# Kernel optimization log

Measured on AMD Instinct MI355X. Metric: run time of the kernel, lower is better.

Reference implementation:

```python
import jax, jax.numpy as jnp
import numpy as np

N, E, V_IN, HID, U_IN, B, MEM = 50000, 800000, 128, 128, 64, 64, 128
CAT = V_IN + HID + U_IN  # 320 == hidden*2 + u_in
ALPHA = 0.5
EPS = 1e-5


def setup_inputs() -> dict:
    key = jax.random.key(0)
    ks = jax.random.split(key, 12)
    x = jax.random.normal(ks[0], (N, V_IN), dtype=jnp.float32)
    edge_index = jax.random.randint(ks[1], (2, E), 0, N, dtype=jnp.int64)
    edge_attr = jax.random.normal(ks[2], (E, HID), dtype=jnp.float32)
    u = jax.random.normal(ks[3], (B, U_IN), dtype=jnp.float32)
    batch = jnp.sort(jax.random.randint(ks[4], (N,), 0, B, dtype=jnp.int64))
    Mk = jax.random.normal(ks[5], (MEM, CAT), dtype=jnp.float32)
    Mv = jax.random.normal(ks[6], (MEM, CAT), dtype=jnp.float32)
    ln_gamma = jnp.ones((CAT,), dtype=jnp.float32)
    ln_beta = jnp.zeros((CAT,), dtype=jnp.float32)
    W1 = jax.random.normal(ks[7], (CAT, HID), dtype=jnp.float32) * (1.0 / np.sqrt(CAT))
    b1 = jnp.zeros((HID,), dtype=jnp.float32)
    W2 = jax.random.normal(ks[8], (HID, HID), dtype=jnp.float32) * (1.0 / np.sqrt(HID))
    b2 = jnp.zeros((HID,), dtype=jnp.float32)
    return {"x": x, "edge_index": edge_index, "edge_attr": edge_attr, "u": u,
            "batch": batch, "Mk": Mk, "Mv": Mv, "ln_gamma": ln_gamma,
            "ln_beta": ln_beta, "W1": W1, "b1": b1, "W2": W2, "b2": b2}


def reference(x, edge_index, edge_attr, u, batch, Mk, Mv, ln_gamma, ln_beta, W1, b1, W2, b2):
    # scatter_add over destination nodes
    agg = jax.ops.segment_sum(edge_attr, edge_index[1], num_segments=N)  # [N, HID]
    out = jnp.concatenate([x, agg, u[batch]], axis=1)  # [N, CAT]
    # LayerNorm over last dim
    mu = jnp.mean(out, axis=-1, keepdims=True)
    var = jnp.var(out, axis=-1, keepdims=True)
    out = (out - mu) * jax.lax.rsqrt(var + EPS) * ln_gamma + ln_beta
    # External attention: [N,CAT] @ [CAT,MEM] -> softmax over MEM -> @ [MEM,CAT]
    scores = jnp.einsum('nc,mc->nm', out, Mk)
    attn = jax.nn.softmax(scores, axis=-1)
    attn_out = jnp.einsum('nm,mc->nc', attn, Mv)
    out = ALPHA * attn_out + (1.0 - ALPHA) * out
    # MLP
    h = jax.nn.relu(out @ W1 + b1)
    return h @ W2 + b2
```

## Files before the change

### kernel.cpp

```cpp
#include <hip/hip_runtime.h>

#define NN   50000
#define EE   800000
#define VIN  128
#define HIDN 128
#define UIN  64
#define MEMN 128
#define CATN 320
#define LN_EPS 1e-5f
#define SCAN_NB 196

typedef __attribute__((ext_vector_type(8))) short short8;
typedef __attribute__((ext_vector_type(4))) float f32x4;
typedef __attribute__((ext_vector_type(4))) unsigned int uint4v;
typedef unsigned short ushort_t;

__device__ inline ushort_t f32_bf16(float f) {
    unsigned u = __float_as_uint(f);
    return (ushort_t)((u + 0x7FFFu + ((u >> 16) & 1u)) >> 16);
}
__device__ inline float bf16_f32(ushort_t h) {
    return __uint_as_float(((unsigned)h) << 16);
}
__device__ inline unsigned pack_hl(float y) {
    unsigned u  = __float_as_uint(y);
    unsigned hi = (u + 0x7FFFu + ((u >> 16) & 1u)) & 0xFFFF0000u;
    float    lo = y - __uint_as_float(hi);
    unsigned v  = __float_as_uint(lo);
    unsigned l16 = ((v + 0x7FFFu + ((v >> 16) & 1u)) >> 16) & 0xFFFFu;
    return hi | l16;
}

__global__ void hist_kernel(const int* __restrict__ edge_dst, int* __restrict__ count)
{
    int gid = blockIdx.x * 256 + threadIdx.x;
    if (gid < EE) atomicAdd(&count[edge_dst[gid]], 1);
}

__global__ void block_sum_kernel(const int* __restrict__ count, int* __restrict__ partials)
{
    __shared__ int s[256];
    const int tid = threadIdx.x;
    const int gid = blockIdx.x * 256 + tid;
    s[tid] = (gid < NN) ? count[gid] : 0;
    __syncthreads();
    for (int off = 128; off >= 1; off >>= 1) {
        if (tid < off) s[tid] += s[tid + off];
        __syncthreads();
    }
    if (tid == 0) partials[blockIdx.x] = s[0];
}

__global__ void scan_partials_kernel(int* __restrict__ partials)
{
    __shared__ int s[256];
    const int tid = threadIdx.x;
    const int v = (tid < SCAN_NB) ? partials[tid] : 0;
    s[tid] = v;
    __syncthreads();
    for (int off = 1; off < 256; off <<= 1) {
        int t = (tid >= off) ? s[tid - off] : 0;
        __syncthreads();
        s[tid] += t;
        __syncthreads();
    }
    if (tid < SCAN_NB) partials[tid] = s[tid] - v;
}

__global__ void make_offsets_kernel(const int* __restrict__ count,
                                    const int* __restrict__ partials,
                                    int* __restrict__ offsets)
{
    __shared__ int s[256];
    const int tid = threadIdx.x;
    const int gid = blockIdx.x * 256 + tid;
    const int v = (gid < NN) ? count[gid] : 0;
    s[tid] = v;
    __syncthreads();
    for (int off = 1; off < 256; off <<= 1) {
        int t = (tid >= off) ? s[tid - off] : 0;
        __syncthreads();
        s[tid] += t;
        __syncthreads();
    }
    if (gid < NN) offsets[gid] = partials[blockIdx.x] + s[tid] - v;
}

__global__ void fill_kernel(const int* __restrict__ edge_dst,
                            const int* __restrict__ offsets,
                            int* __restrict__ cursor,
                            int* __restrict__ bucket)
{
    int gid = blockIdx.x * 256 + threadIdx.x;
    if (gid >= EE) return;
    const int d = edge_dst[gid];
    const int p = atomicAdd(&cursor[d], 1);
    bucket[offsets[d] + p] = gid;
}

__global__ __launch_bounds__(256) void gather_ln_kernel(
    const float* __restrict__ edge_attr,
    const int*   __restrict__ bucket,
    const int*   __restrict__ offsets,
    const int*   __restrict__ count,
    const float* __restrict__ x,
    const float* __restrict__ u,
    const int*   __restrict__ batch,
    const float* __restrict__ gamma,
    const float* __restrict__ beta,
    unsigned*    __restrict__ ln_pk)
{
    const int wid  = (blockIdx.x * 256 + threadIdx.x) >> 6;
    const int lane = threadIdx.x & 63;
    if (wid >= NN) return;

    const int start = offsets[wid];
    const int deg   = count[wid];
    float2 a = make_float2(0.f, 0.f);
    for (int i = 0; i < deg; ++i) {
        const int e = bucket[start + i];
        const float2 v = reinterpret_cast<const float2*>(edge_attr)[e * 64 + lane];
        a.x += v.x;
        a.y += v.y;
    }
    const float2 xv = reinterpret_cast<const float2*>(x)[(size_t)wid * 64 + lane];
    const float  uv = u[batch[wid] * UIN + lane];

    float s = xv.x + xv.y + a.x + a.y + uv;
    float q = xv.x * xv.x + xv.y * xv.y + a.x * a.x + a.y * a.y + uv * uv;
    #pragma unroll
    for (int off = 32; off >= 1; off >>= 1) {
        s += __shfl_xor(s, off);
        q += __shfl_xor(q, off);
    }
    const float mu  = s * (1.0f / CATN);
    const float var = q * (1.0f / CATN) - mu * mu;
    const float rs  = rsqrtf(var + LN_EPS);

    const float2 g0 = reinterpret_cast<const float2*>(gamma)[lane];
    const float2 g1 = reinterpret_cast<const float2*>(gamma)[64 + lane];
    const float  g2 = gamma[256 + lane];
    const float2 t0 = reinterpret_cast<const float2*>(beta)[lane];
    const float2 t1 = reinterpret_cast<const float2*>(beta)[64 + lane];
    const float  t2 = beta[256 + lane];

    unsigned* row = ln_pk + (size_t)wid * CATN;
    uint2 p01, p23;
    p01.x = pack_hl((xv.x - mu) * rs * g0.x + t0.x);
    p01.y = pack_hl((xv.y - mu) * rs * g0.y + t0.y);
    p23.x = pack_hl((a.x - mu) * rs * g1.x + t1.x);
    p23.y = pack_hl((a.y - mu) * rs * g1.y + t1.y);
    reinterpret_cast<uint2*>(row)[lane]       = p01;
    reinterpret_cast<uint2*>(row + 128)[lane] = p23;
    row[256 + lane] = pack_hl((uv - mu) * rs * g2 + t2);
}

__global__ void prep_mk_kernel(const float* __restrict__ Mk,
                               ushort_t* __restrict__ mk_hi, ushort_t* __restrict__ mk_lo)
{
    int i = blockIdx.x * 256 + threadIdx.x;
    if (i < MEMN * CATN) {
        const float f = Mk[i];
        const ushort_t h = f32_bf16(f);
        mk_hi[i] = h;
        mk_lo[i] = f32_bf16(f - bf16_f32(h));
    }
}
__global__ void prep_mvt_kernel(const float* __restrict__ Mv, ushort_t* __restrict__ mv_t)
{
    int i = blockIdx.x * 256 + threadIdx.x;
    if (i < CATN * MEMN) {
        int c = i >> 7, m = i & 127;
        mv_t[i] = f32_bf16(Mv[m * CATN + c]);
    }
}
__global__ void prep_w1t_kernel(const float* __restrict__ W1, ushort_t* __restrict__ w1_t)
{
    int i = blockIdx.x * 256 + threadIdx.x;
    if (i < HIDN * CATN) {
        int n = i / CATN, k = i - n * CATN;
        w1_t[i] = f32_bf16(W1[k * HIDN + n]);
    }
}
__global__ void prep_w2t_kernel(const float* __restrict__ W2, ushort_t* __restrict__ w2_t)
{
    int i = blockIdx.x * 256 + threadIdx.x;
    if (i < HIDN * HIDN) {
        int n = i >> 7, k = i & 127;
        w2_t[i] = f32_bf16(W2[k * HIDN + n]);
    }
}

#define MSTR 328
#define SSTR 132
#define PSTR 136

__global__ __launch_bounds__(256) void node_mfma_kernel(
    const unsigned* __restrict__ ln_pk,
    const ushort_t* __restrict__ mk_hi,
    const ushort_t* __restrict__ mk_lo,
    const ushort_t* __restrict__ mv_t,
    const ushort_t* __restrict__ w1_t,
    const ushort_t* __restrict__ w2_t,
    const float*    __restrict__ b1,
    const float*    __restrict__ b2,
    float*          __restrict__ out)
{
    __shared__ __align__(16) ushort_t s_lnh[32 * MSTR];
    __shared__ __align__(16) ushort_t s_lnl[32 * MSTR];
    __shared__ __align__(16) float    s_S[32 * SSTR];
    __shared__ __align__(16) ushort_t s_P[32 * PSTR];

    const int tid  = threadIdx.x;
    const int wv   = tid >> 6;
    const int lane = tid & 63;
    const int l15  = lane & 15;
    const int l4   = lane >> 4;
    const int node0 = blockIdx.x * 32;

    const f32x4 zero4 = {0.f, 0.f, 0.f, 0.f};

    for (int j = tid; j < 32 * 80; j += 256) {
        const int nl = j / 80;
        const int c0 = (j - nl * 80) * 4;
        int ng = node0 + nl; ng = (ng < NN) ? ng : (NN - 1);
        const uint4v p = *(const uint4v*)(ln_pk + (size_t)ng * CATN + c0);
        ushort_t* ph = s_lnh + nl * MSTR + c0;
        ushort_t* pl = s_lnl + nl * MSTR + c0;
        ph[0] = (ushort_t)(p.x >> 16);  pl[0] = (ushort_t)(p.x & 0xFFFFu);
        ph[1] = (ushort_t)(p.y >> 16);  pl[1] = (ushort_t)(p.y & 0xFFFFu);
        ph[2] = (ushort_t)(p.z >> 16);  pl[2] = (ushort_t)(p.z & 0xFFFFu);
        ph[3] = (ushort_t)(p.w >> 16);  pl[3] = (ushort_t)(p.w & 0xFFFFu);
    }
    __syncthreads();

    {
        f32x4 acc[2][2];
        #pragma unroll
        for (int mt = 0; mt < 2; ++mt)
            #pragma unroll
            for (int nt = 0; nt < 2; ++nt) acc[mt][nt] = zero4;

        for (int kc = 0; kc < 10; ++kc) {
            const int koff = kc * 32 + l4 * 8;
            short8 ah[2], al[2], bh[2], bl[2];
            #pragma unroll
            for (int mt = 0; mt < 2; ++mt) {
                ah[mt] = *(const short8*)(s_lnh + (mt * 16 + l15) * MSTR + koff);
                al[mt] = *(const short8*)(s_lnl + (mt * 16 + l15) * MSTR + koff);
            }
            #pragma unroll
            for (int nt = 0; nt < 2; ++nt) {
                const int mr = (wv * 2 + nt) * 16 + l15;
                bh[nt] = *(const short8*)(mk_hi + (size_t)mr * CATN + koff);
                bl[nt] = *(const short8*)(mk_lo + (size_t)mr * CATN + koff);
            }
            #pragma unroll
            for (int mt = 0; mt < 2; ++mt)
                #pragma unroll
                for (int nt = 0; nt < 2; ++nt) {
                    acc[mt][nt] = __builtin_amdgcn_mfma_f32_16x16x32_bf16(ah[mt], bh[nt], acc[mt][nt], 0, 0, 0);
                    acc[mt][nt] = __builtin_amdgcn_mfma_f32_16x16x32_bf16(ah[mt], bl[nt], acc[mt][nt], 0, 0, 0);
                    acc[mt][nt] = __builtin_amdgcn_mfma_f32_16x16x32_bf16(al[mt], bh[nt], acc[mt][nt], 0, 0, 0);
                }
        }
        #pragma unroll
        for (int mt = 0; mt < 2; ++mt)
            #pragma unroll
            for (int nt = 0; nt < 2; ++nt)
                #pragma unroll
                for (int r = 0; r < 4; ++r)
                    s_S[(mt * 16 + l4 * 4 + r) * SSTR + (wv * 2 + nt) * 16 + l15] = acc[mt][nt][r];
    }
    __syncthreads();

    {
        const int nd = tid >> 3, j = tid & 7;
        const float* row = s_S + nd * SSTR + j * 16;
        float vals[16];
        float mx = -1e30f;
        #pragma unroll
        for (int i = 0; i < 16; ++i) { vals[i] = row[i]; mx = fmaxf(mx, vals[i]); }
        mx = fmaxf(mx, __shfl_xor(mx, 1));
        mx = fmaxf(mx, __shfl_xor(mx, 2));
        mx = fmaxf(mx, __shfl_xor(mx, 4));
        float sm = 0.f;
        #pragma unroll
        for (int i = 0; i < 16; ++i) { vals[i] = __expf(vals[i] - mx); sm += vals[i]; }
        sm += __shfl_xor(sm, 1);
        sm += __shfl_xor(sm, 2);
        sm += __shfl_xor(sm, 4);
        const float inv = 1.f / sm;
        unsigned* prow = (unsigned*)(s_P + nd * PSTR + j * 16);
        #pragma unroll
        for (int i2 = 0; i2 < 8; ++i2) {
            unsigned pk = (unsigned)f32_bf16(vals[2 * i2] * inv) |
                          ((unsigned)f32_bf16(vals[2 * i2 + 1] * inv) << 16);
            prow[i2] = pk;
        }
    }
    __syncthreads();

    {
        f32x4 acc[2][5];
        #pragma unroll
        for (int mt = 0; mt < 2; ++mt)
            #pragma unroll
            for (int nn = 0; nn < 5; ++nn) acc[mt][nn] = zero4;

        for (int kc = 0; kc < 4; ++kc) {
            const int koff = kc * 32 + l4 * 8;
            short8 ap[2];
            #pragma unroll
            for (int mt = 0; mt < 2; ++mt)
                ap[mt] = *(const short8*)(s_P + (mt * 16 + l15) * PSTR + koff);
            short8 bv[5];
            #pragma unroll
            for (int nn = 0; nn < 5; ++nn) {
                const int c = (wv * 5 + nn) * 16 + l15;
                bv[nn] = *(const short8*)(mv_t + (size_t)c * MEMN + koff);
            }
            #pragma unroll
            for (int mt = 0; mt < 2; ++mt)
                #pragma unroll
                for (int nn = 0; nn < 5; ++nn)
                    acc[mt][nn] = __builtin_amdgcn_mfma_f32_16x16x32_bf16(ap[mt], bv[nn], acc[mt][nn], 0, 0, 0);
        }
        #pragma unroll
        for (int mt = 0; mt < 2; ++mt)
            #pragma unroll
            for (int nn = 0; nn < 5; ++nn)
                #pragma unroll
                for (int r = 0; r < 4; ++r) {
                    const int node_l = mt * 16 + l4 * 4 + r;
                    const int c = (wv * 5 + nn) * 16 + l15;
                    const int idx = node_l * MSTR + c;
                    const float lnv = bf16_f32(s_lnh[idx]) + bf16_f32(s_lnl[idx]);
                    s_lnh[idx] = f32_bf16(0.5f * (acc[mt][nn][r] + lnv));
                }
    }
    __syncthreads();

    {
        f32x4 acc[2][2];
        #pragma unroll
        for (int mt = 0; mt < 2; ++mt)
            #pragma unroll
            for (int nt = 0; nt < 2; ++nt) acc[mt][nt] = zero4;

        for (int kc = 0; kc < 10; ++kc) {
            const int koff = kc * 32 + l4 * 8;
            short8 am[2], bw[2];
            #pragma unroll
            for (int mt = 0; mt < 2; ++mt)
                am[mt] = *(const short8*)(s_lnh + (mt * 16 + l15) * MSTR + koff);
            #pragma unroll
            for (int nt = 0; nt < 2; ++nt) {
                const int n = (wv * 2 + nt) * 16 + l15;
                bw[nt] = *(const short8*)(w1_t + (size_t)n * CATN + koff);
            }
            #pragma unroll
            for (int mt = 0; mt < 2; ++mt)
                #pragma unroll
                for (int nt = 0; nt < 2; ++nt)
                    acc[mt][nt] = __builtin_amdgcn_mfma_f32_16x16x32_bf16(am[mt], bw[nt], acc[mt][nt], 0, 0, 0);
        }
        float bb[2];
        #pragma unroll
        for (int nt = 0; nt < 2; ++nt) bb[nt] = b1[(wv * 2 + nt) * 16 + l15];
        __syncthreads();
        #pragma unroll
        for (int mt = 0; mt < 2; ++mt)
            #pragma unroll
            for (int nt = 0; nt < 2; ++nt)
                #pragma unroll
                for (int r = 0; r < 4; ++r) {
                    const int node_l = mt * 16 + l4 * 4 + r;
                    const int col = (wv * 2 + nt) * 16 + l15;
                    s_P[node_l * PSTR + col] = f32_bf16(fmaxf(acc[mt][nt][r] + bb[nt], 0.f));
                }
    }
    __syncthreads();

    {
        f32x4 acc[2][2];
        #pragma unroll
        for (int mt = 0; mt < 2; ++mt)
            #pragma unroll
            for (int nt = 0; nt < 2; ++nt) acc[mt][nt] = zero4;

        for (int kc = 0; kc < 4; ++kc) {
            const int koff = kc * 32 + l4 * 8;
            short8 ah[2], bw[2];
            #pragma unroll
            for (int mt = 0; mt < 2; ++mt)
                ah[mt] = *(const short8*)(s_P + (mt * 16 + l15) * PSTR + koff);
            #pragma unroll
            for (int nt = 0; nt < 2; ++nt) {
                const int n = (wv * 2 + nt) * 16 + l15;
                bw[nt] = *(const short8*)(w2_t + (size_t)n * HIDN + koff);
            }
            #pragma unroll
            for (int mt = 0; mt < 2; ++mt)
                #pragma unroll
                for (int nt = 0; nt < 2; ++nt)
                    acc[mt][nt] = __builtin_amdgcn_mfma_f32_16x16x32_bf16(ah[mt], bw[nt], acc[mt][nt], 0, 0, 0);
        }
        float bb[2];
        #pragma unroll
        for (int nt = 0; nt < 2; ++nt) bb[nt] = b2[(wv * 2 + nt) * 16 + l15];
        #pragma unroll
        for (int mt = 0; mt < 2; ++mt)
            #pragma unroll
            for (int nt = 0; nt < 2; ++nt)
                #pragma unroll
                for (int r = 0; r < 4; ++r) {
                    const int ng = node0 + mt * 16 + l4 * 4 + r;
                    if (ng < NN) {
                        const int col = (wv * 2 + nt) * 16 + l15;
                        out[(size_t)ng * HIDN + col] = acc[mt][nt][r] + bb[nt];
                    }
                }
    }
}

extern "C" void kernel_launch(void* const* d_in, const int* in_sizes, int n_in,
                              void* d_out, int out_size, void* d_ws, size_t ws_size,
                              hipStream_t stream)
{
    const float* x         = (const float*)d_in[0];
    const int*   edge_idx  = (const int*)  d_in[1];
    const float* edge_attr = (const float*)d_in[2];
    const float* u         = (const float*)d_in[3];
    const int*   batch     = (const int*)  d_in[4];
    const float* Mk        = (const float*)d_in[5];
    const float* Mv        = (const float*)d_in[6];
    const float* gamma     = (const float*)d_in[7];
    const float* beta      = (const float*)d_in[8];
    const float* W1        = (const float*)d_in[9];
    const float* b1        = (const float*)d_in[10];
    const float* W2        = (const float*)d_in[11];
    const float* b2        = (const float*)d_in[12];
    float*       out       = (float*)d_out;

    char* w = (char*)d_ws;
    int*   count     = (int*)w;        w += (size_t)NN * sizeof(int);
    int*   cursor    = (int*)w;        w += (size_t)NN * sizeof(int);
    int*   offsets   = (int*)w;        w += (size_t)NN * sizeof(int);
    int*   partials  = (int*)w;        w += 256 * sizeof(int);
    int*   bucket    = (int*)w;        w += (size_t)EE * sizeof(int);
    w = (char*)(((size_t)w + 255) & ~(size_t)255);
    unsigned* ln_pk  = (unsigned*)w;   w += (size_t)NN * CATN * sizeof(unsigned);
    ushort_t* mk_hi  = (ushort_t*)w;   w += (size_t)MEMN * CATN * 2;
    ushort_t* mk_lo  = (ushort_t*)w;   w += (size_t)MEMN * CATN * 2;
    ushort_t* mv_t   = (ushort_t*)w;   w += (size_t)CATN * MEMN * 2;
    ushort_t* w1_t   = (ushort_t*)w;   w += (size_t)HIDN * CATN * 2;
    ushort_t* w2_t   = (ushort_t*)w;   w += (size_t)HIDN * HIDN * 2;

    const int* edge_dst = edge_idx + EE;

    hipMemsetAsync(count, 0, (size_t)2 * NN * sizeof(int), stream);

    const int eb = (EE + 255) / 256;
    hist_kernel<<<eb, 256, 0, stream>>>(edge_dst, count);
    block_sum_kernel<<<SCAN_NB, 256, 0, stream>>>(count, partials);
    scan_partials_kernel<<<1, 256, 0, stream>>>(partials);
    make_offsets_kernel<<<SCAN_NB, 256, 0, stream>>>(count, partials, offsets);
    fill_kernel<<<eb, 256, 0, stream>>>(edge_dst, offsets, cursor, bucket);

    prep_mk_kernel <<<(MEMN * CATN + 255) / 256, 256, 0, stream>>>(Mk, mk_hi, mk_lo);
    prep_mvt_kernel<<<(CATN * MEMN + 255) / 256, 256, 0, stream>>>(Mv, mv_t);
    prep_w1t_kernel<<<(HIDN * CATN + 255) / 256, 256, 0, stream>>>(W1, w1_t);
    prep_w2t_kernel<<<(HIDN * HIDN + 255) / 256, 256, 0, stream>>>(W2, w2_t);

    gather_ln_kernel<<<(NN * 64 + 255) / 256, 256, 0, stream>>>(
        edge_attr, bucket, offsets, count, x, u, batch, gamma, beta, ln_pk);

    node_mfma_kernel<<<(NN + 31) / 32, 256, 0, stream>>>(
        ln_pk, mk_hi, mk_lo, mv_t, w1_t, w2_t, b1, b2, out);
}
```

Measured before the change: 354.1 us.

## Unroll edge gather by four, vectorize LDS split stores, unroll MFMA k-loops

The edge aggregation loop in the gather/LayerNorm kernel is unrolled by four. This keeps four independent edge_attr row loads in flight per wave to hide gather latency. The hi/lo bf16 split stores into shared memory become single 4-wide vector stores instead of scalar ushort writes. Unroll pragmas are added to the MFMA k-loops. The prep kernels are moved without change, and the summation order changes slightly, which alters float rounding.

```diff
diff --git a/kernel.cpp b/kernel.cpp
--- a/kernel.cpp
+++ b/kernel.cpp
@@ -13,6 +13,7 @@
 typedef __attribute__((ext_vector_type(8))) short short8;
 typedef __attribute__((ext_vector_type(4))) float f32x4;
 typedef __attribute__((ext_vector_type(4))) unsigned int uint4v;
+typedef __attribute__((ext_vector_type(4))) unsigned short ushort4v;
 typedef unsigned short ushort_t;
 
 __device__ inline ushort_t f32_bf16(float f) {
@@ -96,6 +97,42 @@
     const int d = edge_dst[gid];
     const int p = atomicAdd(&cursor[d], 1);
     bucket[offsets[d] + p] = gid;
+}
+
+__global__ void prep_mk_kernel(const float* __restrict__ Mk,
+                               ushort_t* __restrict__ mk_hi, ushort_t* __restrict__ mk_lo)
+{
+    int i = blockIdx.x * 256 + threadIdx.x;
+    if (i < MEMN * CATN) {
+        const float f = Mk[i];
+        const ushort_t h = f32_bf16(f);
+        mk_hi[i] = h;
+        mk_lo[i] = f32_bf16(f - bf16_f32(h));
+    }
+}
+__global__ void prep_mvt_kernel(const float* __restrict__ Mv, ushort_t* __restrict__ mv_t)
+{
+    int i = blockIdx.x * 256 + threadIdx.x;
+    if (i < CATN * MEMN) {
+        int c = i >> 7, m = i & 127;
+        mv_t[i] = f32_bf16(Mv[m * CATN + c]);
+    }
+}
+__global__ void prep_w1t_kernel(const float* __restrict__ W1, ushort_t* __restrict__ w1_t)
+{
+    int i = blockIdx.x * 256 + threadIdx.x;
+    if (i < HIDN * CATN) {
+        int n = i / CATN, k = i - n * CATN;
+        w1_t[i] = f32_bf16(W1[k * HIDN + n]);
+    }
+}
+__global__ void prep_w2t_kernel(const float* __restrict__ W2, ushort_t* __restrict__ w2_t)
+{
+    int i = blockIdx.x * 256 + threadIdx.x;
+    if (i < HIDN * HIDN) {
+        int n = i >> 7, k = i & 127;
+        w2_t[i] = f32_bf16(W2[k * HIDN + n]);
+    }
 }
 
 __global__ __launch_bounds__(256) void gather_ln_kernel(
@@ -116,10 +153,25 @@
 
     const int start = offsets[wid];
     const int deg   = count[wid];
+    const float2* ea2 = reinterpret_cast<const float2*>(edge_attr);
     float2 a = make_float2(0.f, 0.f);
-    for (int i = 0; i < deg; ++i) {
+    int i = 0;
+    const int d4 = deg & ~3;
+    for (; i < d4; i += 4) {
+        const int e0 = bucket[start + i];
+        const int e1 = bucket[start + i + 1];
+        const int e2 = bucket[start + i + 2];
+        const int e3 = bucket[start + i + 3];
+        const float2 v0 = ea2[(size_t)e0 * 64 + lane];
+        const float2 v1 = ea2[(size_t)e1 * 64 + lane];
+        const float2 v2 = ea2[(size_t)e2 * 64 + lane];
+        const float2 v3 = ea2[(size_t)e3 * 64 + lane];
+        a.x += (v0.x + v1.x) + (v2.x + v3.x);
+        a.y += (v0.y + v1.y) + (v2.y + v3.y);
+    }
+    for (; i < deg; ++i) {
         const int e = bucket[start + i];
-        const float2 v = reinterpret_cast<const float2*>(edge_attr)[e * 64 + lane];
+        const float2 v = ea2[(size_t)e * 64 + lane];
         a.x += v.x;
         a.y += v.y;
     }
@@ -153,42 +205,6 @@
     reinterpret_cast<uint2*>(row)[lane]       = p01;
     reinterpret_cast<uint2*>(row + 128)[lane] = p23;
     row[256 + lane] = pack_hl((uv - mu) * rs * g2 + t2);
-}
-
-__global__ void prep_mk_kernel(const float* __restrict__ Mk,
-                               ushort_t* __restrict__ mk_hi, ushort_t* __restrict__ mk_lo)
-{
-    int i = blockIdx.x * 256 + threadIdx.x;
-    if (i < MEMN * CATN) {
-        const float f = Mk[i];
-        const ushort_t h = f32_bf16(f);
-        mk_hi[i] = h;
-        mk_lo[i] = f32_bf16(f - bf16_f32(h));
-    }
-}
-__global__ void prep_mvt_kernel(const float* __restrict__ Mv, ushort_t* __restrict__ mv_t)
-{
-    int i = blockIdx.x * 256 + threadIdx.x;
-    if (i < CATN * MEMN) {
-        int c = i >> 7, m = i & 127;
-        mv_t[i] = f32_bf16(Mv[m * CATN + c]);
-    }
-}
-__global__ void prep_w1t_kernel(const float* __restrict__ W1, ushort_t* __restrict__ w1_t)
-{
-    int i = blockIdx.x * 256 + threadIdx.x;
-    if (i < HIDN * CATN) {
-        int n = i / CATN, k = i - n * CATN;
-        w1_t[i] = f32_bf16(W1[k * HIDN + n]);
-    }
-}
-__global__ void prep_w2t_kernel(const float* __restrict__ W2, ushort_t* __restrict__ w2_t)
-{
-    int i = blockIdx.x * 256 + threadIdx.x;
-    if (i < HIDN * HIDN) {
-        int n = i >> 7, k = i & 127;
-        w2_t[i] = f32_bf16(W2[k * HIDN + n]);
-    }
 }
 
 #define MSTR 328
@@ -225,12 +241,13 @@
         const int c0 = (j - nl * 80) * 4;
         int ng = node0 + nl; ng = (ng < NN) ? ng : (NN - 1);
         const uint4v p = *(const uint4v*)(ln_pk + (size_t)ng * CATN + c0);
-        ushort_t* ph = s_lnh + nl * MSTR + c0;
-        ushort_t* pl = s_lnl + nl * MSTR + c0;
-        ph[0] = (ushort_t)(p.x >> 16);  pl[0] = (ushort_t)(p.x & 0xFFFFu);
-        ph[1] = (ushort_t)(p.y >> 16);  pl[1] = (ushort_t)(p.y & 0xFFFFu);
-        ph[2] = (ushort_t)(p.z >> 16);  pl[2] = (ushort_t)(p.z & 0xFFFFu);
-        ph[3] = (ushort_t)(p.w >> 16);  pl[3] = (ushort_t)(p.w & 0xFFFFu);
+        ushort4v h4, l4v;
+        h4.x = (ushort_t)(p.x >> 16);  l4v.x = (ushort_t)(p.x & 0xFFFFu);
+        h4.y = (ushort_t)(p.y >> 16);  l4v.y = (ushort_t)(p.y & 0xFFFFu);
+        h4.z = (ushort_t)(p.z >> 16);  l4v.z = (ushort_t)(p.z & 0xFFFFu);
+        h4.w = (ushort_t)(p.w >> 16);  l4v.w = (ushort_t)(p.w & 0xFFFFu);
+        *(ushort4v*)(s_lnh + nl * MSTR + c0) = h4;
+        *(ushort4v*)(s_lnl + nl * MSTR + c0) = l4v;
     }
     __syncthreads();
 
@@ -241,6 +258,7 @@
             #pragma unroll
             for (int nt = 0; nt < 2; ++nt) acc[mt][nt] = zero4;
 
+        #pragma unroll 2
         for (int kc = 0; kc < 10; ++kc) {
             const int koff = kc * 32 + l4 * 8;
             short8 ah[2], al[2], bh[2], bl[2];
@@ -308,6 +326,7 @@
             #pragma unroll
             for (int nn = 0; nn < 5; ++nn) acc[mt][nn] = zero4;
 
+        #pragma unroll
         for (int kc = 0; kc < 4; ++kc) {
             const int koff = kc * 32 + l4 * 8;
             short8 ap[2];
@@ -348,6 +367,7 @@
             #pragma unroll
             for (int nt = 0; nt < 2; ++nt) acc[mt][nt] = zero4;
 
+        #pragma unroll 2
         for (int kc = 0; kc < 10; ++kc) {
             const int koff = kc * 32 + l4 * 8;
             short8 am[2], bw[2];
@@ -389,6 +409,7 @@
             #pragma unroll
             for (int nt = 0; nt < 2; ++nt) acc[mt][nt] = zero4;
 
+        #pragma unroll
         for (int kc = 0; kc < 4; ++kc) {
             const int koff = kc * 32 + l4 * 8;
             short8 ah[2], bw[2];
```

New measurement: 311.1 us. 1.14x faster.
